# Performance work log

Hardware: AMD Instinct MI355X
Metric: run time of the kernel (lower is better)

The kernel has to match this reference:

```python
import jax, jax.numpy as jnp
import numpy as np

B, T = 2048, 512
INPUT, H, OUT = 5, 32, 2


def _uniform(key, shape, k):
    return jax.random.uniform(key, shape, jnp.float32, -k, k)


def setup_inputs() -> dict:
    key = jax.random.key(0)
    ks = jax.random.split(key, 12)
    k = 1.0 / np.sqrt(H)  # PyTorch LSTM/Linear init scale
    return {
        "x": jax.random.normal(ks[0], (B, T, INPUT), jnp.float32),
        # layer 0 (gate order i, f, g, o as in PyTorch)
        "W_ih0": _uniform(ks[1], (4 * H, INPUT), k),
        "W_hh0": _uniform(ks[2], (4 * H, H), k),
        "b_ih0": _uniform(ks[3], (4 * H,), k),
        "b_hh0": _uniform(ks[4], (4 * H,), k),
        # layer 1
        "W_ih1": _uniform(ks[5], (4 * H, H), k),
        "W_hh1": _uniform(ks[6], (4 * H, H), k),
        "b_ih1": _uniform(ks[7], (4 * H,), k),
        "b_hh1": _uniform(ks[8], (4 * H,), k),
        # final linear head
        "W_fc": _uniform(ks[9], (OUT, H), k),
        "b_fc": _uniform(ks[10], (OUT,), k),
    }


def _lstm_layer(x_seq, W_ih, W_hh, b_ih, b_hh):
    """x_seq: [B, T, D] -> hidden states [B, T, H] and final h [B, H]."""
    b = x_seq.shape[0]
    h_dim = W_hh.shape[1]
    # precompute input contribution for all timesteps: [T, B, 4H]
    xp = (jnp.einsum("btd,gd->btg", x_seq, W_ih) + (b_ih + b_hh)).transpose(1, 0, 2)

    def step(carry, xt):
        h, c = carry
        gates = xt + h @ W_hh.T  # [B, 4H]
        i, f, g, o = jnp.split(gates, 4, axis=-1)
        i = jax.nn.sigmoid(i)
        f = jax.nn.sigmoid(f)
        g = jnp.tanh(g)
        o = jax.nn.sigmoid(o)
        c = f * c + i * g
        h = o * jnp.tanh(c)
        return (h, c), h

    init = (jnp.zeros((b, h_dim), x_seq.dtype), jnp.zeros((b, h_dim), x_seq.dtype))
    (h_last, _), hs = jax.lax.scan(step, init, xp)
    return hs.transpose(1, 0, 2), h_last


def reference(x, W_ih0, W_hh0, b_ih0, b_hh0, W_ih1, W_hh1, b_ih1, b_hh1, W_fc, b_fc):
    hs0, _ = _lstm_layer(x, W_ih0, W_hh0, b_ih0, b_hh0)   # [B, T, H]
    _, h_last = _lstm_layer(hs0, W_ih1, W_hh1, b_ih1, b_hh1)  # [B, H] (== out[:, -1, :])
    return h_last @ W_fc.T + b_fc  # [B, OUT]
```

## Files before the change

### kernel.cpp

```cpp
#include <hip/hip_runtime.h>

typedef float v2f __attribute__((ext_vector_type(2)));

#define T_LEN 512
#define INP 5
#define HID 32

__device__ __forceinline__ v2f pkfma(v2f a, v2f b, v2f c) {
    return __builtin_elementwise_fma(a, b, c);
}

__global__ __launch_bounds__(64, 2) void lstm2_fused(
    const float* __restrict__ x,
    const float* __restrict__ Wih0, const float* __restrict__ Whh0,
    const float* __restrict__ bih0, const float* __restrict__ bhh0,
    const float* __restrict__ Wih1, const float* __restrict__ Whh1,
    const float* __restrict__ bih1, const float* __restrict__ bhh1,
    const float* __restrict__ Wfc,  const float* __restrict__ bfc,
    float* __restrict__ out)
{
    const int b = blockIdx.x;
    const int l = threadIdx.x;
    const int glo = l, ghi = l + 64;
    const bool isIG = (l < 32);
    const int m = l & 31;

    __shared__ __align__(16) float h0s[HID];
    __shared__ __align__(16) float h1s[HID];

    v2f whh0_lo[16], whh0_hi[16], wih1_lo[16], wih1_hi[16], whh1_lo[16], whh1_hi[16];

#define LOADW(dst_lo, dst_hi, W) { \
    const float4* rlo_ = (const float4*)((W) + glo * HID); \
    const float4* rhi_ = (const float4*)((W) + ghi * HID); \
    _Pragma("unroll") \
    for (int r = 0; r < 8; ++r) { \
        float4 a_ = rlo_[r], c_ = rhi_[r]; \
        dst_lo[2*r]   = (v2f){a_.x, a_.y}; \
        dst_lo[2*r+1] = (v2f){a_.z, a_.w}; \
        dst_hi[2*r]   = (v2f){c_.x, c_.y}; \
        dst_hi[2*r+1] = (v2f){c_.z, c_.w}; \
    } }

    LOADW(whh0_lo, whh0_hi, Whh0)
    LOADW(wih1_lo, wih1_hi, Wih1)
    LOADW(whh1_lo, whh1_hi, Whh1)
#undef LOADW

    float wx_lo[INP], wx_hi[INP];
    #pragma unroll
    for (int d = 0; d < INP; ++d) {
        wx_lo[d] = Wih0[glo * INP + d];
        wx_hi[d] = Wih0[ghi * INP + d];
    }

    const float bias0_lo = bih0[glo] + bhh0[glo];
    const float bias0_hi = bih0[ghi] + bhh0[ghi];
    const float bias1_lo = bih1[glo] + bhh1[glo];
    const float bias1_hi = bih1[ghi] + bhh1[ghi];

    const float kk_hi = isIG ? -2.0f : -1.0f;
    const float sc_hi = isIG ?  2.0f :  1.0f;
    const float bb_hi = isIG ? -1.0f :  0.0f;

    float c0 = 0.0f, c1 = 0.0f;
    float h1last = 0.0f;
    if (l < HID) { h0s[l] = 0.0f; h1s[l] = 0.0f; }
    __syncthreads();

    const float* xb = x + (size_t)b * T_LEN * INP;

    for (int t = 0; t < T_LEN; ++t) {
        const float* xp = xb + t * INP;
        const float x0 = xp[0], x1 = xp[1], x2 = xp[2], x3 = xp[3], x4 = xp[4];

        const float4* h04 = (const float4*)h0s;
        const float4* h14 = (const float4*)h1s;

        v2f aL0 = (v2f)0.0f, aL1 = (v2f)0.0f, aH0 = (v2f)0.0f, aH1 = (v2f)0.0f;
        #pragma unroll
        for (int r = 0; r < 8; ++r) {
            float4 hq = h04[r];
            v2f hp0 = (v2f){hq.x, hq.y};
            v2f hp1 = (v2f){hq.z, hq.w};
            aL0 = pkfma(whh0_lo[2*r],   hp0, aL0);
            aL1 = pkfma(whh0_lo[2*r+1], hp1, aL1);
            aH0 = pkfma(whh0_hi[2*r],   hp0, aH0);
            aH1 = pkfma(whh0_hi[2*r+1], hp1, aH1);
        }
        float gl = bias0_lo + ((aL0.x + aL1.x) + (aL0.y + aL1.y));
        float gh = bias0_hi + ((aH0.x + aH1.x) + (aH0.y + aH1.y));
        gl = fmaf(wx_lo[0], x0, gl); gl = fmaf(wx_lo[1], x1, gl);
        gl = fmaf(wx_lo[2], x2, gl); gl = fmaf(wx_lo[3], x3, gl);
        gl = fmaf(wx_lo[4], x4, gl);
        gh = fmaf(wx_hi[0], x0, gh); gh = fmaf(wx_hi[1], x1, gh);
        gh = fmaf(wx_hi[2], x2, gh); gh = fmaf(wx_hi[3], x3, gh);
        gh = fmaf(wx_hi[4], x4, gh);

        float actL = __builtin_amdgcn_rcpf(1.0f + __expf(-gl));
        float actH = fmaf(sc_hi, __builtin_amdgcn_rcpf(1.0f + __expf(kk_hi * gh)), bb_hi);
        float actLs = __shfl_xor(actL, 32);
        float actHs = __shfl_xor(actH, 32);
        float i_ = isIG ? actL  : actLs;
        float f_ = isIG ? actLs : actL;
        float g_ = isIG ? actH  : actHs;
        float o_ = isIG ? actHs : actH;
        c0 = fmaf(f_, c0, i_ * g_);
        float th0 = fmaf(2.0f, __builtin_amdgcn_rcpf(1.0f + __expf(-2.0f * c0)), -1.0f);
        float h0new = o_ * th0;
        if (l < HID) h0s[l] = h0new;
        __syncthreads();

        v2f bL0 = (v2f)0.0f, bL1 = (v2f)0.0f, bH0 = (v2f)0.0f, bH1 = (v2f)0.0f;
        #pragma unroll
        for (int r = 0; r < 8; ++r) {
            float4 hq = h04[r];
            v2f hp0 = (v2f){hq.x, hq.y};
            v2f hp1 = (v2f){hq.z, hq.w};
            bL0 = pkfma(wih1_lo[2*r],   hp0, bL0);
            bL1 = pkfma(wih1_lo[2*r+1], hp1, bL1);
            bH0 = pkfma(wih1_hi[2*r],   hp0, bH0);
            bH1 = pkfma(wih1_hi[2*r+1], hp1, bH1);
        }
        #pragma unroll
        for (int r = 0; r < 8; ++r) {
            float4 hq = h14[r];
            v2f hp0 = (v2f){hq.x, hq.y};
            v2f hp1 = (v2f){hq.z, hq.w};
            bL0 = pkfma(whh1_lo[2*r],   hp0, bL0);
            bL1 = pkfma(whh1_lo[2*r+1], hp1, bL1);
            bH0 = pkfma(whh1_hi[2*r],   hp0, bH0);
            bH1 = pkfma(whh1_hi[2*r+1], hp1, bH1);
        }
        float gl1 = bias1_lo + ((bL0.x + bL1.x) + (bL0.y + bL1.y));
        float gh1 = bias1_hi + ((bH0.x + bH1.x) + (bH0.y + bH1.y));

        float actL1 = __builtin_amdgcn_rcpf(1.0f + __expf(-gl1));
        float actH1 = fmaf(sc_hi, __builtin_amdgcn_rcpf(1.0f + __expf(kk_hi * gh1)), bb_hi);
        float actL1s = __shfl_xor(actL1, 32);
        float actH1s = __shfl_xor(actH1, 32);
        float i1 = isIG ? actL1  : actL1s;
        float f1 = isIG ? actL1s : actL1;
        float g1 = isIG ? actH1  : actH1s;
        float o1 = isIG ? actH1s : actH1;
        c1 = fmaf(f1, c1, i1 * g1);
        float th1 = fmaf(2.0f, __builtin_amdgcn_rcpf(1.0f + __expf(-2.0f * c1)), -1.0f);
        h1last = o1 * th1;
        if (l < HID) h1s[l] = h1last;
        __syncthreads();
    }

    float p0 = isIG ? (Wfc[m]       * h1last) : 0.0f;
    float p1 = isIG ? (Wfc[HID + m] * h1last) : 0.0f;
    #pragma unroll
    for (int off = 32; off >= 1; off >>= 1) {
        p0 += __shfl_xor(p0, off);
        p1 += __shfl_xor(p1, off);
    }
    if (l == 0) {
        out[2 * b + 0] = p0 + bfc[0];
        out[2 * b + 1] = p1 + bfc[1];
    }
}

extern "C" void kernel_launch(void* const* d_in, const int* in_sizes, int n_in,
                              void* d_out, int out_size, void* d_ws, size_t ws_size,
                              hipStream_t stream) {
    const float* x    = (const float*)d_in[0];
    const float* Wih0 = (const float*)d_in[1];
    const float* Whh0 = (const float*)d_in[2];
    const float* bih0 = (const float*)d_in[3];
    const float* bhh0 = (const float*)d_in[4];
    const float* Wih1 = (const float*)d_in[5];
    const float* Whh1 = (const float*)d_in[6];
    const float* bih1 = (const float*)d_in[7];
    const float* bhh1 = (const float*)d_in[8];
    const float* Wfc  = (const float*)d_in[9];
    const float* bfc  = (const float*)d_in[10];
    float* out = (float*)d_out;

    const int nb = in_sizes[0] / (T_LEN * INP);
    lstm2_fused<<<dim3(nb), dim3(64), 0, stream>>>(
        x, Wih0, Whh0, bih0, bhh0, Wih1, Whh1, bih1, bhh1, Wfc, bfc, out);
}
```

Before: 478.8 us.

## Pipeline the two LSTM layers across three wavefronts with double-buffered hidden state

Each block now runs three wavefronts: one computes layer 0, one computes the layer-1 input projection from the previous layer-0 state, and one runs the layer-1 recurrence. Hidden states and projections pass between them through double-buffered shared memory, with one barrier per pipeline step. This splits the serial per-step chain across wavefronts and cuts per-thread weight registers from six matrices to two, which may allow higher occupancy. In exchange the block is three times larger and each step's latency is set by the slowest stage plus a block-wide barrier.

Result: slower. 602.8 us (+25.9%).

```diff
diff --git a/kernel.cpp b/kernel.cpp
--- a/kernel.cpp
+++ b/kernel.cpp
@@ -10,7 +10,7 @@
     return __builtin_elementwise_fma(a, b, c);
 }
 
-__global__ __launch_bounds__(64, 2) void lstm2_fused(
+__global__ __launch_bounds__(192, 4) void lstm2_pipe(
     const float* __restrict__ x,
     const float* __restrict__ Wih0, const float* __restrict__ Whh0,
     const float* __restrict__ bih0, const float* __restrict__ bhh0,
@@ -19,148 +19,154 @@
     const float* __restrict__ Wfc,  const float* __restrict__ bfc,
     float* __restrict__ out)
 {
-    const int b = blockIdx.x;
-    const int l = threadIdx.x;
+    const int b   = blockIdx.x;
+    const int tid = threadIdx.x;
+    const int wid = tid >> 6;
+    const int l   = tid & 63;
     const int glo = l, ghi = l + 64;
     const bool isIG = (l < 32);
-    const int m = l & 31;
 
-    __shared__ __align__(16) float h0s[HID];
-    __shared__ __align__(16) float h1s[HID];
+    __shared__ __align__(16) float h0buf[2][HID];
+    __shared__ __align__(16) float h1buf[2][HID];
+    __shared__ __align__(16) float p1buf[2][4 * HID];
 
-    v2f whh0_lo[16], whh0_hi[16], wih1_lo[16], wih1_hi[16], whh1_lo[16], whh1_hi[16];
+    if (tid < HID) { h0buf[1][tid] = 0.0f; h1buf[1][tid] = 0.0f; }
 
-#define LOADW(dst_lo, dst_hi, W) { \
-    const float4* rlo_ = (const float4*)((W) + glo * HID); \
-    const float4* rhi_ = (const float4*)((W) + ghi * HID); \
-    _Pragma("unroll") \
-    for (int r = 0; r < 8; ++r) { \
-        float4 a_ = rlo_[r], c_ = rhi_[r]; \
-        dst_lo[2*r]   = (v2f){a_.x, a_.y}; \
-        dst_lo[2*r+1] = (v2f){a_.z, a_.w}; \
-        dst_hi[2*r]   = (v2f){c_.x, c_.y}; \
-        dst_hi[2*r+1] = (v2f){c_.z, c_.w}; \
-    } }
-
-    LOADW(whh0_lo, whh0_hi, Whh0)
-    LOADW(wih1_lo, wih1_hi, Wih1)
-    LOADW(whh1_lo, whh1_hi, Whh1)
-#undef LOADW
-
-    float wx_lo[INP], wx_hi[INP];
-    #pragma unroll
-    for (int d = 0; d < INP; ++d) {
-        wx_lo[d] = Wih0[glo * INP + d];
-        wx_hi[d] = Wih0[ghi * INP + d];
+    const float* WA = (wid == 0) ? Whh0 : (wid == 1 ? Wih1 : Whh1);
+    v2f wlo[16], whi[16];
+    {
+        const float4* rlo = (const float4*)(WA + glo * HID);
+        const float4* rhi = (const float4*)(WA + ghi * HID);
+        #pragma unroll
+        for (int r = 0; r < 8; ++r) {
+            float4 a_ = rlo[r], c_ = rhi[r];
+            wlo[2*r]   = (v2f){a_.x, a_.y};
+            wlo[2*r+1] = (v2f){a_.z, a_.w};
+            whi[2*r]   = (v2f){c_.x, c_.y};
+            whi[2*r+1] = (v2f){c_.z, c_.w};
+        }
     }
 
-    const float bias0_lo = bih0[glo] + bhh0[glo];
-    const float bias0_hi = bih0[ghi] + bhh0[ghi];
-    const float bias1_lo = bih1[glo] + bhh1[glo];
-    const float bias1_hi = bih1[ghi] + bhh1[ghi];
+    float biaslo = 0.0f, biashi = 0.0f;
+    if (wid == 0) { biaslo = bih0[glo] + bhh0[glo]; biashi = bih0[ghi] + bhh0[ghi]; }
+    if (wid == 1) { biaslo = bih1[glo] + bhh1[glo]; biashi = bih1[ghi] + bhh1[ghi]; }
+
+    v2f wxlo01 = (v2f)0.0f, wxlo23 = (v2f)0.0f, wxhi01 = (v2f)0.0f, wxhi23 = (v2f)0.0f;
+    float wxlo4 = 0.0f, wxhi4 = 0.0f;
+    if (wid == 0) {
+        const float* rl = Wih0 + glo * INP;
+        const float* rh = Wih0 + ghi * INP;
+        wxlo01 = (v2f){rl[0], rl[1]}; wxlo23 = (v2f){rl[2], rl[3]}; wxlo4 = rl[4];
+        wxhi01 = (v2f){rh[0], rh[1]}; wxhi23 = (v2f){rh[2], rh[3]}; wxhi4 = rh[4];
+    }
 
     const float kk_hi = isIG ? -2.0f : -1.0f;
     const float sc_hi = isIG ?  2.0f :  1.0f;
     const float bb_hi = isIG ? -1.0f :  0.0f;
 
-    float c0 = 0.0f, c1 = 0.0f;
-    float h1last = 0.0f;
-    if (l < HID) { h0s[l] = 0.0f; h1s[l] = 0.0f; }
+    float cst = 0.0f;
+    float hlast = 0.0f;
+
+    const float* xb = x + (size_t)b * T_LEN * INP;
+    float xa0 = 0.f, xa1 = 0.f, xa2 = 0.f, xa3 = 0.f, xa4 = 0.f;
+    if (wid == 0) { xa0 = xb[0]; xa1 = xb[1]; xa2 = xb[2]; xa3 = xb[3]; xa4 = xb[4]; }
+
     __syncthreads();
 
-    const float* xb = x + (size_t)b * T_LEN * INP;
+#define DOT16(HSRC, GL, GH) { \
+    v2f aL0 = (v2f)0.0f, aL1 = (v2f)0.0f, aH0 = (v2f)0.0f, aH1 = (v2f)0.0f; \
+    const float4* h4_ = (const float4*)(HSRC); \
+    _Pragma("unroll") \
+    for (int r = 0; r < 8; ++r) { \
+        float4 hq = h4_[r]; \
+        v2f hp0 = (v2f){hq.x, hq.y}; \
+        v2f hp1 = (v2f){hq.z, hq.w}; \
+        aL0 = pkfma(wlo[2*r],   hp0, aL0); \
+        aL1 = pkfma(wlo[2*r+1], hp1, aL1); \
+        aH0 = pkfma(whi[2*r],   hp0, aH0); \
+        aH1 = pkfma(whi[2*r+1], hp1, aH1); \
+    } \
+    GL = (aL0.x + aL1.x) + (aL0.y + aL1.y); \
+    GH = (aH0.x + aH1.x) + (aH0.y + aH1.y); \
+}
 
-    for (int t = 0; t < T_LEN; ++t) {
-        const float* xp = xb + t * INP;
-        const float x0 = xp[0], x1 = xp[1], x2 = xp[2], x3 = xp[3], x4 = xp[4];
+    for (int s = 0; s < T_LEN + 2; ++s) {
+        if (wid == 0) {
+            if (s < T_LEN) {
+                float gl, gh;
+                DOT16(h0buf[(s + 1) & 1], gl, gh);
+                v2f xv01 = (v2f){xa0, xa1}, xv23 = (v2f){xa2, xa3};
+                v2f tl = pkfma(wxlo01, xv01, pkfma(wxlo23, xv23, (v2f)0.0f));
+                v2f th_ = pkfma(wxhi01, xv01, pkfma(wxhi23, xv23, (v2f)0.0f));
+                gl += biaslo + tl.x + tl.y + wxlo4 * xa4;
+                gh += biashi + th_.x + th_.y + wxhi4 * xa4;
 
-        const float4* h04 = (const float4*)h0s;
-        const float4* h14 = (const float4*)h1s;
+                float actL = __builtin_amdgcn_rcpf(1.0f + __expf(-gl));
+                float actH = fmaf(sc_hi, __builtin_amdgcn_rcpf(1.0f + __expf(kk_hi * gh)), bb_hi);
+                float actLs = __shfl_xor(actL, 32);
+                float actHs = __shfl_xor(actH, 32);
+                float i_ = isIG ? actL  : actLs;
+                float f_ = isIG ? actLs : actL;
+                float g_ = isIG ? actH  : actHs;
+                float o_ = isIG ? actHs : actH;
+                cst = fmaf(f_, cst, i_ * g_);
+                float th0 = fmaf(2.0f, __builtin_amdgcn_rcpf(1.0f + __expf(-2.0f * cst)), -1.0f);
+                float hnew = o_ * th0;
+                if (l < HID) h0buf[s & 1][l] = hnew;
+                if (s + 1 < T_LEN) {
+                    const float* xp = xb + (s + 1) * INP;
+                    xa0 = xp[0]; xa1 = xp[1]; xa2 = xp[2]; xa3 = xp[3]; xa4 = xp[4];
+                }
+            }
+        } else if (wid == 1) {
+            if (s >= 1 && s <= T_LEN) {
+                float pl, ph;
+                DOT16(h0buf[(s + 1) & 1], pl, ph);
+                pl += biaslo; ph += biashi;
+                p1buf[(s + 1) & 1][glo] = pl;
+                p1buf[(s + 1) & 1][ghi] = ph;
+            }
+        } else {
+            if (s >= 2) {
+                const int t2 = s - 2;
+                float gl = p1buf[t2 & 1][glo];
+                float gh = p1buf[t2 & 1][ghi];
+                float dl, dh;
+                DOT16(h1buf[(t2 + 1) & 1], dl, dh);
+                gl += dl; gh += dh;
 
-        v2f aL0 = (v2f)0.0f, aL1 = (v2f)0.0f, aH0 = (v2f)0.0f, aH1 = (v2f)0.0f;
-        #pragma unroll
-        for (int r = 0; r < 8; ++r) {
-            float4 hq = h04[r];
-            v2f hp0 = (v2f){hq.x, hq.y};
-            v2f hp1 = (v2f){hq.z, hq.w};
-            aL0 = pkfma(whh0_lo[2*r],   hp0, aL0);
-            aL1 = pkfma(whh0_lo[2*r+1], hp1, aL1);
-            aH0 = pkfma(whh0_hi[2*r],   hp0, aH0);
-            aH1 = pkfma(whh0_hi[2*r+1], hp1, aH1);
+                float actL = __builtin_amdgcn_rcpf(1.0f + __expf(-gl));
+                float actH = fmaf(sc_hi, __builtin_amdgcn_rcpf(1.0f + __expf(kk_hi * gh)), bb_hi);
+                float actLs = __shfl_xor(actL, 32);
+                float actHs = __shfl_xor(actH, 32);
+                float i_ = isIG ? actL  : actLs;
+                float f_ = isIG ? actLs : actL;
+                float g_ = isIG ? actH  : actHs;
+                float o_ = isIG ? actHs : actH;
+                cst = fmaf(f_, cst, i_ * g_);
+                float th1 = fmaf(2.0f, __builtin_amdgcn_rcpf(1.0f + __expf(-2.0f * cst)), -1.0f);
+                hlast = o_ * th1;
+                if (l < HID) h1buf[t2 & 1][l] = hlast;
+            }
         }
-        float gl = bias0_lo + ((aL0.x + aL1.x) + (aL0.y + aL1.y));
-        float gh = bias0_hi + ((aH0.x + aH1.x) + (aH0.y + aH1.y));
-        gl = fmaf(wx_lo[0], x0, gl); gl = fmaf(wx_lo[1], x1, gl);
-        gl = fmaf(wx_lo[2], x2, gl); gl = fmaf(wx_lo[3], x3, gl);
-        gl = fmaf(wx_lo[4], x4, gl);
-        gh = fmaf(wx_hi[0], x0, gh); gh = fmaf(wx_hi[1], x1, gh);
-        gh = fmaf(wx_hi[2], x2, gh); gh = fmaf(wx_hi[3], x3, gh);
-        gh = fmaf(wx_hi[4], x4, gh);
-
-        float actL = __builtin_amdgcn_rcpf(1.0f + __expf(-gl));
-        float actH = fmaf(sc_hi, __builtin_amdgcn_rcpf(1.0f + __expf(kk_hi * gh)), bb_hi);
-        float actLs = __shfl_xor(actL, 32);
-        float actHs = __shfl_xor(actH, 32);
-        float i_ = isIG ? actL  : actLs;
-        float f_ = isIG ? actLs : actL;
-        float g_ = isIG ? actH  : actHs;
-        float o_ = isIG ? actHs : actH;
-        c0 = fmaf(f_, c0, i_ * g_);
-        float th0 = fmaf(2.0f, __builtin_amdgcn_rcpf(1.0f + __expf(-2.0f * c0)), -1.0f);
-        float h0new = o_ * th0;
-        if (l < HID) h0s[l] = h0new;
-        __syncthreads();
-
-        v2f bL0 = (v2f)0.0f, bL1 = (v2f)0.0f, bH0 = (v2f)0.0f, bH1 = (v2f)0.0f;
-        #pragma unroll
-        for (int r = 0; r < 8; ++r) {
-            float4 hq = h04[r];
-            v2f hp0 = (v2f){hq.x, hq.y};
-            v2f hp1 = (v2f){hq.z, hq.w};
-            bL0 = pkfma(wih1_lo[2*r],   hp0, bL0);
-            bL1 = pkfma(wih1_lo[2*r+1], hp1, bL1);
-            bH0 = pkfma(wih1_hi[2*r],   hp0, bH0);
-            bH1 = pkfma(wih1_hi[2*r+1], hp1, bH1);
-        }
-        #pragma unroll
-        for (int r = 0; r < 8; ++r) {
-            float4 hq = h14[r];
-            v2f hp0 = (v2f){hq.x, hq.y};
-            v2f hp1 = (v2f){hq.z, hq.w};
-            bL0 = pkfma(whh1_lo[2*r],   hp0, bL0);
-            bL1 = pkfma(whh1_lo[2*r+1], hp1, bL1);
-            bH0 = pkfma(whh1_hi[2*r],   hp0, bH0);
-            bH1 = pkfma(whh1_hi[2*r+1], hp1, bH1);
-        }
-        float gl1 = bias1_lo + ((bL0.x + bL1.x) + (bL0.y + bL1.y));
-        float gh1 = bias1_hi + ((bH0.x + bH1.x) + (bH0.y + bH1.y));
-
-        float actL1 = __builtin_amdgcn_rcpf(1.0f + __expf(-gl1));
-        float actH1 = fmaf(sc_hi, __builtin_amdgcn_rcpf(1.0f + __expf(kk_hi * gh1)), bb_hi);
-        float actL1s = __shfl_xor(actL1, 32);
-        float actH1s = __shfl_xor(actH1, 32);
-        float i1 = isIG ? actL1  : actL1s;
-        float f1 = isIG ? actL1s : actL1;
-        float g1 = isIG ? actH1  : actH1s;
-        float o1 = isIG ? actH1s : actH1;
-        c1 = fmaf(f1, c1, i1 * g1);
-        float th1 = fmaf(2.0f, __builtin_amdgcn_rcpf(1.0f + __expf(-2.0f * c1)), -1.0f);
-        h1last = o1 * th1;
-        if (l < HID) h1s[l] = h1last;
         __syncthreads();
     }
 
-    float p0 = isIG ? (Wfc[m]       * h1last) : 0.0f;
-    float p1 = isIG ? (Wfc[HID + m] * h1last) : 0.0f;
-    #pragma unroll
-    for (int off = 32; off >= 1; off >>= 1) {
-        p0 += __shfl_xor(p0, off);
-        p1 += __shfl_xor(p1, off);
+    if (wid == 2) {
+        const int m = l & 31;
+        float p0 = isIG ? (Wfc[m]       * hlast) : 0.0f;
+        float p1 = isIG ? (Wfc[HID + m] * hlast) : 0.0f;
+        #pragma unroll
+        for (int off = 32; off >= 1; off >>= 1) {
+            p0 += __shfl_xor(p0, off);
+            p1 += __shfl_xor(p1, off);
+        }
+        if (l == 0) {
+            out[2 * b + 0] = p0 + bfc[0];
+            out[2 * b + 1] = p1 + bfc[1];
+        }
     }
-    if (l == 0) {
-        out[2 * b + 0] = p0 + bfc[0];
-        out[2 * b + 1] = p1 + bfc[1];
-    }
+#undef DOT16
 }
 
 extern "C" void kernel_launch(void* const* d_in, const int* in_sizes, int n_in,
@@ -180,6 +186,6 @@
     float* out = (float*)d_out;
 
     const int nb = in_sizes[0] / (T_LEN * INP);
-    lstm2_fused<<<dim3(nb), dim3(64), 0, stream>>>(
+    lstm2_pipe<<<dim3(nb), dim3(192), 0, stream>>>(
         x, Wih0, Whh0, bih0, bhh0, Wih1, Whh1, bih1, bhh1, Wfc, bfc, out);
 }
```
